# Optimization experiments

Hardware: AMD Instinct MI355X
Metric: run time of the kernel (lower is better)

## Reference

```python
import jax, jax.numpy as jnp
import numpy as np

B, C, H, W = 32, 512, 32, 32
INNER = C // 8


def setup_inputs() -> dict:
    key = jax.random.key(0)
    k_x, k_f, k_g, k_h = jax.random.split(key, 4)
    x = jax.random.normal(k_x, (B, C, H, W), dtype=jnp.float32)
    # 1x1 Conv1d weights (bias=False) are plain [out, in] matrices.
    s_in = 1.0 / np.sqrt(C)
    Wf = jax.random.uniform(k_f, (INNER, C), dtype=jnp.float32, minval=-s_in, maxval=s_in)
    Wg = jax.random.uniform(k_g, (INNER, C), dtype=jnp.float32, minval=-s_in, maxval=s_in)
    Wh = jax.random.uniform(k_h, (C, C), dtype=jnp.float32, minval=-s_in, maxval=s_in)
    return {"x": x, "Wf": Wf, "Wg": Wg, "Wh": Wh}


def reference(x, Wf, Wg, Wh):
    b, c = x.shape[0], x.shape[1]
    xf = x.reshape(b, c, -1)                       # [B, C, N]
    f = jnp.einsum('ic,bcn->bin', Wf, xf)          # [B, inner, N]
    g = jnp.einsum('ic,bcn->bin', Wg, xf)          # [B, inner, N]
    h = jnp.einsum('oc,bcn->bon', Wh, xf)          # [B, C, N]
    sim = jnp.einsum('bin,bim->bnm', f, g)         # f^T g -> [B, N, N]
    beta = jax.nn.softmax(sim, axis=1)             # softmax over the f-index axis (dim=1)
    o = jnp.einsum('bcn,bnm->bcm', h, beta)        # [B, C, N]
    return o
```

## Files before the change

### kernel.cpp

```cpp
#include <hip/hip_runtime.h>
#include <stdint.h>

#define CDIM 512
#define NPIX 1024
#define IDIM 64

#define WS_BATCH (65536 + 65536 + 524288)
#define XT_OFF   ((size_t)32 * WS_BATCH)
#define XT_ELEMS ((size_t)32 * 1024 * 512)
#define WH_OFF   (XT_OFF + XT_ELEMS)
#define P_OFF    XT_OFF
#define P_ELEMS  ((size_t)32 * 1024 * 1024)
#define LP_OFF   (P_OFF + P_ELEMS)

typedef __bf16 bf16x8 __attribute__((ext_vector_type(8)));
typedef _Float16 f16x8 __attribute__((ext_vector_type(8)));
typedef float f32x4 __attribute__((ext_vector_type(4)));

__device__ __forceinline__ unsigned short f2bf(float f) {
    union { float f; uint32_t u; } v; v.f = f;
    uint32_t u = v.u;
    u += 0x7fffu + ((u >> 16) & 1u);
    return (unsigned short)(u >> 16);
}

__device__ __forceinline__ f32x4 mfma_bf(bf16x8 a, bf16x8 b, f32x4 c) {
    return __builtin_amdgcn_mfma_f32_16x16x32_bf16(a, b, c, 0, 0, 0);
}
__device__ __forceinline__ f32x4 mfma_h(f16x8 a, f16x8 b, f32x4 c) {
    return __builtin_amdgcn_mfma_f32_16x16x32_f16(a, b, c, 0, 0, 0);
}
__device__ __forceinline__ void gld_lds16(const void* g, void* l) {
    __builtin_amdgcn_global_load_lds(
        (const __attribute__((address_space(1))) unsigned int*)g,
        (__attribute__((address_space(3))) unsigned int*)l,
        16, 0, 0);
}
__device__ __forceinline__ void barrier_mem() {
    asm volatile("" ::: "memory");
    __builtin_amdgcn_s_barrier();
    asm volatile("" ::: "memory");
}
__device__ __forceinline__ int swz(int by) { return by ^ (((by >> 7) & 3) << 4); }

__global__ __launch_bounds__(256) void wcvt(
    const float* __restrict__ Wf, const float* __restrict__ Wg,
    const float* __restrict__ Wh, _Float16* __restrict__ wh)
{
    int e = (blockIdx.x * 256 + threadIdx.x) * 4;
    int r = e >> 9, k = e & 511;
    const float* src;
    if (r < 64)       src = Wf + (size_t)r * 512 + k;
    else if (r < 128) src = Wg + (size_t)(r - 64) * 512 + k;
    else              src = Wh + (size_t)(r - 128) * 512 + k;
    float4 v = *(const float4*)src;
    _Float16 h4[4] = {(_Float16)v.x, (_Float16)v.y, (_Float16)v.z, (_Float16)v.w};
    *(ushort4*)(wh + e) = *(ushort4*)h4;
}

__global__ __launch_bounds__(256) void xcvt(
    const float* __restrict__ x, _Float16* __restrict__ xT)
{
    __shared__ _Float16 tile[64][72];
    const int b = blockIdx.z, c0 = blockIdx.y * 64, n0 = blockIdx.x * 64;
    const int t = threadIdx.x;
    const float* xb = x + ((size_t)b * CDIM + c0) * NPIX + n0;
    #pragma unroll
    for (int p = 0; p < 4; ++p) {
        int ci = p * 16 + (t >> 4);
        int nj = (t & 15) * 4;
        float4 v = *(const float4*)(xb + (size_t)ci * NPIX + nj);
        tile[nj + 0][ci] = (_Float16)v.x;
        tile[nj + 1][ci] = (_Float16)v.y;
        tile[nj + 2][ci] = (_Float16)v.z;
        tile[nj + 3][ci] = (_Float16)v.w;
    }
    __syncthreads();
    _Float16* dst = xT + ((size_t)b * NPIX + n0) * CDIM + c0;
    #pragma unroll
    for (int p = 0; p < 2; ++p) {
        int n  = p * 32 + (t >> 3);
        int cc = (t & 7) * 8;
        ushort4 a  = *(ushort4*)&tile[n][cc];
        ushort4 bq = *(ushort4*)&tile[n][cc + 4];
        *(ushort4*)(dst + (size_t)n * CDIM + cc)     = a;
        *(ushort4*)(dst + (size_t)n * CDIM + cc + 4) = bq;
    }
}

__global__ __launch_bounds__(256, 4) void fg_mfma(
    const _Float16* __restrict__ wh, const _Float16* __restrict__ xT,
    unsigned short* __restrict__ ws)
{
    const int orig = blockIdx.x;
    const int work = (orig & 7) * 32 + (orig >> 3);
    const int b    = work >> 3;
    const int tn   = work & 7;

    const int t = threadIdx.x, lane = t & 63, w = t >> 6;
    const int lr = lane & 15, lg = lane >> 4;
    const int wr = w >> 1, wc = w & 1;

    __shared__ _Float16 Abuf[2][128 * 32];
    __shared__ _Float16 Bbuf[2][128 * 32];

    const _Float16* Ag = wh;
    const _Float16* Bg = xT + ((size_t)b * NPIX + tn * 128) * CDIM;

    int offA[4], offB[4];
    #pragma unroll
    for (int mf = 0; mf < 4; ++mf)
        offA[mf] = swz((wr * 64 + mf * 16 + lr) * 64 + lg * 16);
    #pragma unroll
    for (int nf = 0; nf < 4; ++nf)
        offB[nf] = swz((wc * 64 + nf * 16 + lr) * 64 + lg * 16);

    f32x4 acc[4][4];
    #pragma unroll
    for (int i = 0; i < 4; ++i)
        #pragma unroll
        for (int j = 0; j < 4; ++j) acc[i][j] = (f32x4){0.f, 0.f, 0.f, 0.f};

    auto stage = [&](int buf, int k0) {
        #pragma unroll
        for (int p = 0; p < 2; ++p) {
            int q = p * 256 + t;
            gld_lds16(Ag + (size_t)(q >> 2) * CDIM + k0 + ((q & 3) ^ ((q >> 3) & 3)) * 8,
                      (char*)&Abuf[buf][0] + q * 16);
        }
        #pragma unroll
        for (int p = 0; p < 2; ++p) {
            int q = p * 256 + t;
            gld_lds16(Bg + (size_t)(q >> 2) * CDIM + k0 + ((q & 3) ^ ((q >> 3) & 3)) * 8,
                      (char*)&Bbuf[buf][0] + q * 16);
        }
    };

    stage(0, 0);
    stage(1, 32);

    #pragma unroll 1
    for (int ks = 0; ks < 16; ++ks) {
        const int cur = ks & 1;
        if (ks < 15) asm volatile("s_waitcnt vmcnt(4)" ::: "memory");
        else         asm volatile("s_waitcnt vmcnt(0)" ::: "memory");
        barrier_mem();

        const char* Ab = (const char*)&Abuf[cur][0];
        const char* Bb = (const char*)&Bbuf[cur][0];
        f16x8 af[4];
        #pragma unroll
        for (int mf = 0; mf < 4; ++mf)
            af[mf] = *(const f16x8*)(Ab + offA[mf]);
        #pragma unroll
        for (int nf = 0; nf < 4; ++nf) {
            f16x8 bv = *(const f16x8*)(Bb + offB[nf]);
            #pragma unroll
            for (int mf = 0; mf < 4; ++mf)
                acc[mf][nf] = mfma_h(af[mf], bv, acc[mf][nf]);
        }

        barrier_mem();
        if (ks + 2 < 16) stage(cur, (ks + 2) * 32);
    }

    unsigned short* base = ws + (size_t)b * WS_BATCH;
    const int nbase = tn * 128 + wc * 64;
    unsigned short* dst = base + (wr ? 65536 : 0);
    #pragma unroll
    for (int mf = 0; mf < 4; ++mf) {
        const int i0 = mf * 16 + lg * 4;
        #pragma unroll
        for (int nf = 0; nf < 4; ++nf) {
            int n = nbase + nf * 16 + lr;
            ushort4 v;
            v.x = f2bf(acc[mf][nf][0]); v.y = f2bf(acc[mf][nf][1]);
            v.z = f2bf(acc[mf][nf][2]); v.w = f2bf(acc[mf][nf][3]);
            *(ushort4*)(dst + (size_t)n * 64 + i0) = v;
        }
    }
}

__global__ __launch_bounds__(512, 2) void h_mfma(
    const _Float16* __restrict__ wh, const _Float16* __restrict__ xT,
    unsigned short* __restrict__ ws)
{
    const int orig = blockIdx.x;
    const int work = (orig & 7) * 32 + (orig >> 3);
    const int b    = work >> 3;
    const int tile = work & 7;
    const int m0   = (tile >> 2) * 256;
    const int n0   = (tile & 3) * 256;

    const int t = threadIdx.x, lane = t & 63, w = t >> 6;
    const int lr = lane & 15, lg = lane >> 4;
    const int wr = w >> 2, wc = w & 3;

    __shared__ __align__(16) char smem[131072];

    const _Float16* Ag = wh + (size_t)(128 + m0) * CDIM;
    const _Float16* Bg = xT + ((size_t)b * NPIX + n0) * CDIM;

    const int sk0 = ((lg) ^ (lr & 7)) * 16;
    const int sk1 = ((4 + lg) ^ (lr & 7)) * 16;
    const int rAbase = (wr * 128 + lr) * 128;
    const int rBbase = (wc * 64 + lr) * 128;

    f32x4 acc[8][4];
    #pragma unroll
    for (int i = 0; i < 8; ++i)
        #pragma unroll
        for (int j = 0; j < 4; ++j) acc[i][j] = (f32x4){0.f, 0.f, 0.f, 0.f};

    auto stage_half = [&](int buf, int isB, int half, int kt) {
        const _Float16* G = isB ? Bg : Ag;
        char* L = smem + isB * 65536 + buf * 32768 + half * 16384;
        #pragma unroll
        for (int l = 0; l < 2; ++l) {
            int q = l * 512 + t;
            gld_lds16(G + (size_t)(half * 128 + (q >> 3)) * CDIM + kt * 64
                        + (((q & 7) ^ ((q >> 3) & 7)) * 8),
                      L + q * 16);
        }
    };

    stage_half(0, 0, 0, 0); stage_half(0, 0, 1, 0);
    stage_half(0, 1, 0, 0); stage_half(0, 1, 1, 0);
    stage_half(1, 1, 0, 1); stage_half(1, 1, 1, 1);
    asm volatile("s_waitcnt vmcnt(4)" ::: "memory");
    barrier_mem();

    f16x8 bfr[4][2];

    #pragma unroll 1
    for (int j = 0; j < 4; ++j) {
        const bool nl = (j < 3);
        #pragma unroll
        for (int grp = 0; grp < 2; ++grp) {
            const char* Abase = smem + grp * 32768;
            const char* Bbase = smem + 65536 + grp * 32768;
            #pragma unroll
            for (int p = 0; p < 4; ++p) {
                if (p == 0) {
                    #pragma unroll
                    for (int nf = 0; nf < 4; ++nf) {
                        bfr[nf][0] = *(const f16x8*)(Bbase + rBbase + nf * 2048 + sk0);
                        bfr[nf][1] = *(const f16x8*)(Bbase + rBbase + nf * 2048 + sk1);
                    }
                }
                f16x8 af[2][2];
                #pragma unroll
                for (int e = 0; e < 2; ++e) {
                    af[e][0] = *(const f16x8*)(Abase + rAbase + (p * 2 + e) * 2048 + sk0);
                    af[e][1] = *(const f16x8*)(Abase + rAbase + (p * 2 + e) * 2048 + sk1);
                }
                if (grp == 0) {
                    if (p == 0) stage_half(1, 0, 0, 2 * j + 1);
                    if (p == 1) stage_half(1, 0, 1, 2 * j + 1);
                    if (p == 2 && nl) stage_half(0, 1, 0, 2 * j + 2);
                    if (p == 3 && nl) stage_half(0, 1, 1, 2 * j + 2);
                } else {
                    if (p == 0 && nl) stage_half(0, 0, 0, 2 * j + 2);
                    if (p == 1 && nl) stage_half(0, 0, 1, 2 * j + 2);
                    if (p == 2 && nl) stage_half(1, 1, 0, 2 * j + 3);
                    if (p == 3 && nl) stage_half(1, 1, 1, 2 * j + 3);
                }
                if (p == 3) {
                    if (nl) asm volatile("s_waitcnt vmcnt(4)" ::: "memory");
                    else    asm volatile("s_waitcnt vmcnt(0)" ::: "memory");
                }
                barrier_mem();
                __builtin_amdgcn_s_setprio(1);
                #pragma unroll
                for (int ks = 0; ks < 2; ++ks)
                    #pragma unroll
                    for (int e = 0; e < 2; ++e)
                        #pragma unroll
                        for (int nf = 0; nf < 4; ++nf)
                            acc[p * 2 + e][nf] =
                                mfma_h(af[e][ks], bfr[nf][ks], acc[p * 2 + e][nf]);
                __builtin_amdgcn_s_setprio(0);
            }
        }
    }

    unsigned short* hd = ws + (size_t)b * WS_BATCH + 131072;
    #pragma unroll
    for (int mf = 0; mf < 8; ++mf)
        #pragma unroll
        for (int nf = 0; nf < 4; ++nf) {
            int n = n0 + wc * 64 + nf * 16 + lr;
            #pragma unroll
            for (int j = 0; j < 4; ++j) {
                int c = m0 + wr * 128 + mf * 16 + lg * 4 + j;
                hd[(size_t)c * NPIX + n] = f2bf(acc[mf][nf][j]);
            }
        }
}

__global__ __launch_bounds__(256, 3) void attn_sm(
    const unsigned short* __restrict__ ws, unsigned short* __restrict__ P,
    float* __restrict__ Lp)
{
    const int orig = blockIdx.x;
    const int work = (orig & 7) * 256 + (orig >> 3);
    const int b    = work >> 6;
    const int tile = work & 63;
    const int mt = tile >> 2, nt = tile & 3;
    const int m0 = mt * 64, n0 = nt * 256;

    const int t = threadIdx.x, lane = t & 63, w = t >> 6;
    const int lr = lane & 15, lg = lane >> 4;

    const unsigned short* fT = ws + (size_t)b * WS_BATCH;
    const unsigned short* gT = fT + 65536;

    __shared__ unsigned short Ab[2][64 * 32];
    __shared__ unsigned short Bb[2][256 * 32];
    __shared__ float red[4][64];
    __shared__ unsigned short rp[4][16][72];

    #pragma unroll
    for (int kc = 0; kc < 2; ++kc) {
        {
            int q = t;
            gld_lds16(gT + (size_t)(m0 + (q >> 2)) * 64 + kc * 32 + ((q & 3) ^ ((q >> 3) & 3)) * 8,
                      (char*)&Ab[kc][0] + q * 16);
        }
        #pragma unroll
        for (int p = 0; p < 4; ++p) {
            int q = p * 256 + t;
            gld_lds16(fT + (size_t)(n0 + (q >> 2)) * 64 + kc * 32 + ((q & 3) ^ ((q >> 3) & 3)) * 8,
                      (char*)&Bb[kc][0] + q * 16);
        }
    }
    __syncthreads();

    int offA[4], offB[4];
    #pragma unroll
    for (int mf = 0; mf < 4; ++mf)
        offA[mf] = swz((mf * 16 + lr) * 64 + lg * 16);
    #pragma unroll
    for (int nf = 0; nf < 4; ++nf)
        offB[nf] = swz((w * 64 + nf * 16 + lr) * 64 + lg * 16);

    f32x4 acc[4][4];
    #pragma unroll
    for (int i = 0; i < 4; ++i)
        #pragma unroll
        for (int j = 0; j < 4; ++j) acc[i][j] = (f32x4){0.f, 0.f, 0.f, 0.f};

    #pragma unroll
    for (int kc = 0; kc < 2; ++kc) {
        const char* Abc = (const char*)&Ab[kc][0];
        const char* Bbc = (const char*)&Bb[kc][0];
        bf16x8 af[4];
        #pragma unroll
        for (int mf = 0; mf < 4; ++mf)
            af[mf] = *(const bf16x8*)(Abc + offA[mf]);
        #pragma unroll
        for (int nf = 0; nf < 4; ++nf) {
            bf16x8 bv = *(const bf16x8*)(Bbc + offB[nf]);
            #pragma unroll
            for (int mf = 0; mf < 4; ++mf)
                acc[mf][nf] = mfma_bf(af[mf], bv, acc[mf][nf]);
        }
    }

    #pragma unroll
    for (int mf = 0; mf < 4; ++mf) {
        #pragma unroll
        for (int j = 0; j < 4; ++j) {
            float s = 0.f;
            #pragma unroll
            for (int nf = 0; nf < 4; ++nf) {
                float e = __expf(acc[mf][nf][j]);
                acc[mf][nf][j] = e;
                s += e;
            }
            s += __shfl_xor(s, 1);
            s += __shfl_xor(s, 2);
            s += __shfl_xor(s, 4);
            s += __shfl_xor(s, 8);
            if (lr == 0) red[w][mf * 16 + lg * 4 + j] = s;
        }
    }
    __syncthreads();
    if (t < 64) {
        float s = red[0][t] + red[1][t] + red[2][t] + red[3][t];
        Lp[(size_t)nt * 32768 + (size_t)b * 1024 + m0 + t] = s;
    }

    unsigned short* Pb = P + (size_t)b * NPIX * NPIX;
    #pragma unroll
    for (int mf = 0; mf < 4; ++mf) {
        #pragma unroll
        for (int nf = 0; nf < 4; ++nf)
            #pragma unroll
            for (int j = 0; j < 4; ++j)
                rp[w][lg * 4 + j][nf * 16 + lr] = f2bf(acc[mf][nf][j]);
        #pragma unroll
        for (int ii = 0; ii < 2; ++ii) {
            int row = ii * 8 + (lane >> 3);
            int ch  = lane & 7;
            ushort4 v0 = *(ushort4*)&rp[w][row][ch * 8];
            ushort4 v1 = *(ushort4*)&rp[w][row][ch * 8 + 4];
            unsigned short* dst = Pb + (size_t)(m0 + mf * 16 + row) * NPIX
                                     + n0 + w * 64 + ch * 8;
            *(ushort4*)(dst)     = v0;
            *(ushort4*)(dst + 4) = v1;
        }
    }
}

__global__ __launch_bounds__(512, 2) void attn_pv(
    const unsigned short* __restrict__ P, const unsigned short* __restrict__ ws,
    const float* __restrict__ Lp, float* __restrict__ out)
{
    const int orig = blockIdx.x;
    const int work = (orig & 7) * 32 + (orig >> 3);
    const int b    = work >> 3;
    const int tile = work & 7;
    const int m0   = (tile >> 1) * 256;
    const int c0   = (tile & 1) * 256;

    const int t = threadIdx.x, lane = t & 63, w = t >> 6;
    const int lr = lane & 15, lg = lane >> 4;
    const int wr = w >> 2, wc = w & 3;

    __shared__ __align__(16) char smem[131072];

    const unsigned short* Ag = P + ((size_t)b * NPIX + m0) * NPIX;
    const unsigned short* Bg = ws + (size_t)b * WS_BATCH + 131072 + (size_t)c0 * NPIX;

    const int sk0 = ((lg) ^ (lr & 7)) * 16;
    const int sk1 = ((4 + lg) ^ (lr & 7)) * 16;
    const int rAbase = (wr * 128 + lr) * 128;
    const int rBbase = (wc * 64 + lr) * 128;

    f32x4 acc[8][4];
    #pragma unroll
    for (int i = 0; i < 8; ++i)
        #pragma unroll
        for (int j = 0; j < 4; ++j) acc[i][j] = (f32x4){0.f, 0.f, 0.f, 0.f};

    auto stage_half = [&](int buf, int isB, int half, int kt) {
        const unsigned short* G = isB ? Bg : Ag;
        char* L = smem + isB * 65536 + buf * 32768 + half * 16384;
        #pragma unroll
        for (int l = 0; l < 2; ++l) {
            int q = l * 512 + t;
            gld_lds16(G + (size_t)(half * 128 + (q >> 3)) * NPIX + kt * 64
                        + (((q & 7) ^ ((q >> 3) & 7)) * 8),
                      L + q * 16);
        }
    };

    stage_half(0, 0, 0, 0); stage_half(0, 0, 1, 0);
    stage_half(0, 1, 0, 0); stage_half(0, 1, 1, 0);
    stage_half(1, 1, 0, 1); stage_half(1, 1, 1, 1);
    asm volatile("s_waitcnt vmcnt(4)" ::: "memory");
    barrier_mem();

    bf16x8 bfr[4][2];

    #pragma unroll 1
    for (int j = 0; j < 8; ++j) {
        const bool nl = (j < 7);
        #pragma unroll
        for (int grp = 0; grp < 2; ++grp) {
            const char* Abase = smem + grp * 32768;
            const char* Bbase = smem + 65536 + grp * 32768;
            #pragma unroll
            for (int p = 0; p < 4; ++p) {
                if (p == 0) {
                    #pragma unroll
                    for (int nf = 0; nf < 4; ++nf) {
                        bfr[nf][0] = *(const bf16x8*)(Bbase + rBbase + nf * 2048 + sk0);
                        bfr[nf][1] = *(const bf16x8*)(Bbase + rBbase + nf * 2048 + sk1);
                    }
                }
                bf16x8 af[2][2];
                #pragma unroll
                for (int e = 0; e < 2; ++e) {
                    af[e][0] = *(const bf16x8*)(Abase + rAbase + (p * 2 + e) * 2048 + sk0);
                    af[e][1] = *(const bf16x8*)(Abase + rAbase + (p * 2 + e) * 2048 + sk1);
                }
                if (grp == 0) {
                    if (p == 0) stage_half(1, 0, 0, 2 * j + 1);
                    if (p == 1) stage_half(1, 0, 1, 2 * j + 1);
                    if (p == 2 && nl) stage_half(0, 1, 0, 2 * j + 2);
                    if (p == 3 && nl) stage_half(0, 1, 1, 2 * j + 2);
                } else {
                    if (p == 0 && nl) stage_half(0, 0, 0, 2 * j + 2);
                    if (p == 1 && nl) stage_half(0, 0, 1, 2 * j + 2);
                    if (p == 2 && nl) stage_half(1, 1, 0, 2 * j + 3);
                    if (p == 3 && nl) stage_half(1, 1, 1, 2 * j + 3);
                }
                if (p == 3) {
                    if (nl) asm volatile("s_waitcnt vmcnt(4)" ::: "memory");
                    else    asm volatile("s_waitcnt vmcnt(0)" ::: "memory");
                }
                barrier_mem();
                __builtin_amdgcn_s_setprio(1);
                #pragma unroll
                for (int ks = 0; ks < 2; ++ks)
                    #pragma unroll
                    for (int e = 0; e < 2; ++e)
                        #pragma unroll
                        for (int nf = 0; nf < 4; ++nf)
                            acc[p * 2 + e][nf] =
                                mfma_bf(af[e][ks], bfr[nf][ks], acc[p * 2 + e][nf]);
                __builtin_amdgcn_s_setprio(0);
            }
        }
    }

    #pragma unroll
    for (int mf = 0; mf < 8; ++mf) {
        const size_t mi = (size_t)b * 1024 + m0 + wr * 128 + mf * 16 + lg * 4;
        f32x4 L = *(const f32x4*)&Lp[mi]
                + *(const f32x4*)&Lp[32768 + mi]
                + *(const f32x4*)&Lp[65536 + mi]
                + *(const f32x4*)&Lp[98304 + mi];
        f32x4 rinv;
        #pragma unroll
        for (int j = 0; j < 4; ++j) rinv[j] = 1.0f / L[j];
        #pragma unroll
        for (int nf = 0; nf < 4; ++nf) {
            f32x4 o = acc[mf][nf] * rinv;
            int c = c0 + wc * 64 + nf * 16 + lr;
            int m = m0 + wr * 128 + mf * 16 + lg * 4;
            *(f32x4*)(out + ((size_t)b * CDIM + c) * NPIX + m) = o;
        }
    }
}

extern "C" void kernel_launch(void* const* d_in, const int* in_sizes, int n_in,
                              void* d_out, int out_size, void* d_ws, size_t ws_size,
                              hipStream_t stream) {
    const float* x  = (const float*)d_in[0];
    const float* Wf = (const float*)d_in[1];
    const float* Wg = (const float*)d_in[2];
    const float* Wh = (const float*)d_in[3];
    unsigned short* ws = (unsigned short*)d_ws;
    _Float16* xT = (_Float16*)(ws + XT_OFF);
    _Float16* wh = (_Float16*)(ws + WH_OFF);
    unsigned short* P = ws + P_OFF;
    float* Lp = (float*)(ws + LP_OFF);
    float* out = (float*)d_out;

    wcvt<<<320, 256, 0, stream>>>(Wf, Wg, Wh, wh);
    xcvt<<<dim3(16, 8, 32), 256, 0, stream>>>(x, xT);
    fg_mfma<<<256, 256, 0, stream>>>(wh, xT, ws);
    h_mfma<<<256, 512, 0, stream>>>(wh, xT, ws);
    attn_sm<<<2048, 256, 0, stream>>>(ws, P, Lp);
    attn_pv<<<256, 512, 0, stream>>>(P, ws, Lp, out);
}
```

Measured before the change: 121.3 us.

## Fuse softmax numerator recompute into PV kernel, eliminating materialized P matrix

The first attention kernel now only computes the column-sum normalizers. The PV kernel recomputes f^T g tiles per 64-pixel chunk, exponentiates them into a shared-memory bf16 tile, and multiplies by h directly. This removes writing and re-reading the full 32x1024x1024 bf16 probability matrix through HBM. In exchange it recomputes the similarity GEMM and exp, uses about 152KB LDS per block (one block per CU), and adds two barriers per K step.

```diff
diff --git a/kernel.cpp b/kernel.cpp
--- a/kernel.cpp
+++ b/kernel.cpp
@@ -9,9 +9,8 @@
 #define XT_OFF   ((size_t)32 * WS_BATCH)
 #define XT_ELEMS ((size_t)32 * 1024 * 512)
 #define WH_OFF   (XT_OFF + XT_ELEMS)
-#define P_OFF    XT_OFF
 #define P_ELEMS  ((size_t)32 * 1024 * 1024)
-#define LP_OFF   (P_OFF + P_ELEMS)
+#define LP_OFF   (XT_OFF + P_ELEMS)
 
 typedef __bf16 bf16x8 __attribute__((ext_vector_type(8)));
 typedef _Float16 f16x8 __attribute__((ext_vector_type(8)));
@@ -298,9 +297,8 @@
         }
 }
 
-__global__ __launch_bounds__(256, 3) void attn_sm(
-    const unsigned short* __restrict__ ws, unsigned short* __restrict__ P,
-    float* __restrict__ Lp)
+__global__ __launch_bounds__(256, 3) void attn_lp(
+    const unsigned short* __restrict__ ws, float* __restrict__ Lp)
 {
     const int orig = blockIdx.x;
     const int work = (orig & 7) * 256 + (orig >> 3);
@@ -318,7 +316,6 @@
     __shared__ unsigned short Ab[2][64 * 32];
     __shared__ unsigned short Bb[2][256 * 32];
     __shared__ float red[4][64];
-    __shared__ unsigned short rp[4][16][72];
 
     #pragma unroll
     for (int kc = 0; kc < 2; ++kc) {
@@ -373,11 +370,8 @@
         for (int j = 0; j < 4; ++j) {
             float s = 0.f;
             #pragma unroll
-            for (int nf = 0; nf < 4; ++nf) {
-                float e = __expf(acc[mf][nf][j]);
-                acc[mf][nf][j] = e;
-                s += e;
-            }
+            for (int nf = 0; nf < 4; ++nf)
+                s += __expf(acc[mf][nf][j]);
             s += __shfl_xor(s, 1);
             s += __shfl_xor(s, 2);
             s += __shfl_xor(s, 4);
@@ -390,32 +384,11 @@
         float s = red[0][t] + red[1][t] + red[2][t] + red[3][t];
         Lp[(size_t)nt * 32768 + (size_t)b * 1024 + m0 + t] = s;
     }
-
-    unsigned short* Pb = P + (size_t)b * NPIX * NPIX;
-    #pragma unroll
-    for (int mf = 0; mf < 4; ++mf) {
-        #pragma unroll
-        for (int nf = 0; nf < 4; ++nf)
-            #pragma unroll
-            for (int j = 0; j < 4; ++j)
-                rp[w][lg * 4 + j][nf * 16 + lr] = f2bf(acc[mf][nf][j]);
-        #pragma unroll
-        for (int ii = 0; ii < 2; ++ii) {
-            int row = ii * 8 + (lane >> 3);
-            int ch  = lane & 7;
-            ushort4 v0 = *(ushort4*)&rp[w][row][ch * 8];
-            ushort4 v1 = *(ushort4*)&rp[w][row][ch * 8 + 4];
-            unsigned short* dst = Pb + (size_t)(m0 + mf * 16 + row) * NPIX
-                                     + n0 + w * 64 + ch * 8;
-            *(ushort4*)(dst)     = v0;
-            *(ushort4*)(dst + 4) = v1;
-        }
-    }
-}
-
-__global__ __launch_bounds__(512, 2) void attn_pv(
-    const unsigned short* __restrict__ P, const unsigned short* __restrict__ ws,
-    const float* __restrict__ Lp, float* __restrict__ out)
+}
+
+__global__ __launch_bounds__(512, 2) void attn_fused(
+    const unsigned short* __restrict__ ws, const float* __restrict__ Lp,
+    float* __restrict__ out)
 {
     const int orig = blockIdx.x;
     const int work = (orig & 7) * 32 + (orig >> 3);
@@ -426,17 +399,18 @@
 
     const int t = threadIdx.x, lane = t & 63, w = t >> 6;
     const int lr = lane & 15, lg = lane >> 4;
-    const int wr = w >> 2, wc = w & 3;
-
-    __shared__ __align__(16) char smem[131072];
-
-    const unsigned short* Ag = P + ((size_t)b * NPIX + m0) * NPIX;
-    const unsigned short* Bg = ws + (size_t)b * WS_BATCH + 131072 + (size_t)c0 * NPIX;
+    const int wr = w >> 2;
+    const int wq = w & 3;
+
+    const unsigned short* fT = ws + (size_t)b * WS_BATCH;
+    const unsigned short* gT = fT + 65536;
+    const unsigned short* hg = fT + 131072;
+
+    __shared__ __align__(16) char smem[155648];
+    unsigned short* Pl = (unsigned short*)(smem + 114688);
 
     const int sk0 = ((lg) ^ (lr & 7)) * 16;
     const int sk1 = ((4 + lg) ^ (lr & 7)) * 16;
-    const int rAbase = (wr * 128 + lr) * 128;
-    const int rBbase = (wc * 64 + lr) * 128;
 
     f32x4 acc[8][4];
     #pragma unroll
@@ -444,76 +418,98 @@
         #pragma unroll
         for (int j = 0; j < 4; ++j) acc[i][j] = (f32x4){0.f, 0.f, 0.f, 0.f};
 
-    auto stage_half = [&](int buf, int isB, int half, int kt) {
-        const unsigned short* G = isB ? Bg : Ag;
-        char* L = smem + isB * 65536 + buf * 32768 + half * 16384;
-        #pragma unroll
-        for (int l = 0; l < 2; ++l) {
+    auto stage_g = [&]() {
+        #pragma unroll
+        for (int l = 0; l < 4; ++l) {
             int q = l * 512 + t;
-            gld_lds16(G + (size_t)(half * 128 + (q >> 3)) * NPIX + kt * 64
-                        + (((q & 7) ^ ((q >> 3) & 7)) * 8),
-                      L + q * 16);
+            gld_lds16(gT + (size_t)(m0 + (q >> 3)) * 64 + (((q & 7) ^ ((q >> 3) & 7)) * 8),
+                      smem + q * 16);
         }
     };
-
-    stage_half(0, 0, 0, 0); stage_half(0, 0, 1, 0);
-    stage_half(0, 1, 0, 0); stage_half(0, 1, 1, 0);
-    stage_half(1, 1, 0, 1); stage_half(1, 1, 1, 1);
-    asm volatile("s_waitcnt vmcnt(4)" ::: "memory");
+    auto stage_f = [&](int buf, int nt) {
+        int q = t;
+        gld_lds16(fT + (size_t)(nt * 64 + (q >> 3)) * 64 + (((q & 7) ^ ((q >> 3) & 7)) * 8),
+                  smem + 32768 + buf * 8192 + q * 16);
+    };
+    auto stage_h = [&](int buf, int nt) {
+        #pragma unroll
+        for (int l = 0; l < 4; ++l) {
+            int q = l * 512 + t;
+            gld_lds16(hg + (size_t)(c0 + (q >> 3)) * NPIX + nt * 64
+                         + (((q & 7) ^ ((q >> 3) & 7)) * 8),
+                      smem + 49152 + buf * 32768 + q * 16);
+        }
+    };
+
+    stage_g();
+    stage_f(0, 0);
+    stage_h(0, 0);
+    stage_f(1, 1);
+    asm volatile("s_waitcnt vmcnt(1)" ::: "memory");
     barrier_mem();
 
-    bf16x8 bfr[4][2];
-
     #pragma unroll 1
-    for (int j = 0; j < 8; ++j) {
-        const bool nl = (j < 7);
-        #pragma unroll
-        for (int grp = 0; grp < 2; ++grp) {
-            const char* Abase = smem + grp * 32768;
-            const char* Bbase = smem + 65536 + grp * 32768;
-            #pragma unroll
-            for (int p = 0; p < 4; ++p) {
-                if (p == 0) {
+    for (int nt = 0; nt < 16; ++nt) {
+        if (nt + 1 < 16) stage_h((nt + 1) & 1, nt + 1);
+
+        const char* fb = smem + 32768 + (nt & 1) * 8192;
+        bf16x8 qb0 = *(const bf16x8*)(fb + (wq * 16 + lr) * 128 + sk0);
+        bf16x8 qb1 = *(const bf16x8*)(fb + (wq * 16 + lr) * 128 + sk1);
+        f32x4 sacc[8];
+        #pragma unroll
+        for (int mf = 0; mf < 8; ++mf) {
+            const char* ga = smem + (wr * 128 + mf * 16 + lr) * 128;
+            bf16x8 a0 = *(const bf16x8*)(ga + sk0);
+            bf16x8 a1 = *(const bf16x8*)(ga + sk1);
+            f32x4 z = {0.f, 0.f, 0.f, 0.f};
+            z = mfma_bf(a0, qb0, z);
+            sacc[mf] = mfma_bf(a1, qb1, z);
+        }
+        #pragma unroll
+        for (int mf = 0; mf < 8; ++mf) {
+            const int row = wr * 128 + mf * 16 + lg * 4;
+            #pragma unroll
+            for (int j = 0; j < 4; ++j)
+                Pl[(row + j) * 80 + wq * 16 + lr] = f2bf(__expf(sacc[mf][j]));
+        }
+        asm volatile("s_waitcnt lgkmcnt(0)" ::: "memory");
+        barrier_mem();
+
+        if (nt + 2 < 16) stage_f(nt & 1, nt + 2);
+
+        if (nt < 14)       asm volatile("s_waitcnt vmcnt(5)" ::: "memory");
+        else if (nt == 14) asm volatile("s_waitcnt vmcnt(4)" ::: "memory");
+        else               asm volatile("s_waitcnt vmcnt(0)" ::: "memory");
+
+        const char* hb_ = smem + 49152 + (nt & 1) * 32768;
+        bf16x8 hb[4][2];
+        #pragma unroll
+        for (int nf = 0; nf < 4; ++nf) {
+            hb[nf][0] = *(const bf16x8*)(hb_ + (wq * 64 + nf * 16 + lr) * 128 + sk0);
+            hb[nf][1] = *(const bf16x8*)(hb_ + (wq * 64 + nf * 16 + lr) * 128 + sk1);
+        }
+        __builtin_amdgcn_s_setprio(1);
+        #pragma unroll
+        for (int p = 0; p < 4; ++p) {
+            bf16x8 af[2][2];
+            #pragma unroll
+            for (int e = 0; e < 2; ++e) {
+                const char* pa = (const char*)Pl + (wr * 128 + (p * 2 + e) * 16 + lr) * 160;
+                af[e][0] = *(const bf16x8*)(pa + lg * 16);
+                af[e][1] = *(const bf16x8*)(pa + 64 + lg * 16);
+            }
+            #pragma unroll
+            for (int ks = 0; ks < 2; ++ks)
+                #pragma unroll
+                for (int e = 0; e < 2; ++e)
                     #pragma unroll
-                    for (int nf = 0; nf < 4; ++nf) {
-                        bfr[nf][0] = *(const bf16x8*)(Bbase + rBbase + nf * 2048 + sk0);
-                        bfr[nf][1] = *(const bf16x8*)(Bbase + rBbase + nf * 2048 + sk1);
-                    }
-                }
-                bf16x8 af[2][2];
-                #pragma unroll
-                for (int e = 0; e < 2; ++e) {
-                    af[e][0] = *(const bf16x8*)(Abase + rAbase + (p * 2 + e) * 2048 + sk0);
-                    af[e][1] = *(const bf16x8*)(Abase + rAbase + (p * 2 + e) * 2048 + sk1);
-                }
-                if (grp == 0) {
-                    if (p == 0) stage_half(1, 0, 0, 2 * j + 1);
-                    if (p == 1) stage_half(1, 0, 1, 2 * j + 1);
-                    if (p == 2 && nl) stage_half(0, 1, 0, 2 * j + 2);
-                    if (p == 3 && nl) stage_half(0, 1, 1, 2 * j + 2);
-                } else {
-                    if (p == 0 && nl) stage_half(0, 0, 0, 2 * j + 2);
-                    if (p == 1 && nl) stage_half(0, 0, 1, 2 * j + 2);
-                    if (p == 2 && nl) stage_half(1, 1, 0, 2 * j + 3);
-                    if (p == 3 && nl) stage_half(1, 1, 1, 2 * j + 3);
-                }
-                if (p == 3) {
-                    if (nl) asm volatile("s_waitcnt vmcnt(4)" ::: "memory");
-                    else    asm volatile("s_waitcnt vmcnt(0)" ::: "memory");
-                }
-                barrier_mem();
-                __builtin_amdgcn_s_setprio(1);
-                #pragma unroll
-                for (int ks = 0; ks < 2; ++ks)
-                    #pragma unroll
-                    for (int e = 0; e < 2; ++e)
-                        #pragma unroll
-                        for (int nf = 0; nf < 4; ++nf)
-                            acc[p * 2 + e][nf] =
-                                mfma_bf(af[e][ks], bfr[nf][ks], acc[p * 2 + e][nf]);
-                __builtin_amdgcn_s_setprio(0);
-            }
-        }
+                    for (int nf = 0; nf < 4; ++nf)
+                        acc[p * 2 + e][nf] =
+                            mfma_bf(af[e][ks], hb[nf][ks], acc[p * 2 + e][nf]);
+        }
+        __builtin_amdgcn_s_setprio(0);
+        asm volatile("s_waitcnt lgkmcnt(0)" ::: "memory");
+        barrier_mem();
     }
 
     #pragma unroll
@@ -529,7 +525,7 @@
         #pragma unroll
         for (int nf = 0; nf < 4; ++nf) {
             f32x4 o = acc[mf][nf] * rinv;
-            int c = c0 + wc * 64 + nf * 16 + lr;
+            int c = c0 + wq * 64 + nf * 16 + lr;
             int m = m0 + wr * 128 + mf * 16 + lg * 4;
             *(f32x4*)(out + ((size_t)b * CDIM + c) * NPIX + m) = o;
         }
@@ -546,7 +542,6 @@
     unsigned short* ws = (unsigned short*)d_ws;
     _Float16* xT = (_Float16*)(ws + XT_OFF);
     _Float16* wh = (_Float16*)(ws + WH_OFF);
-    unsigned short* P = ws + P_OFF;
     float* Lp = (float*)(ws + LP_OFF);
     float* out = (float*)d_out;
 
@@ -554,6 +549,6 @@
     xcvt<<<dim3(16, 8, 32), 256, 0, stream>>>(x, xT);
     fg_mfma<<<256, 256, 0, stream>>>(wh, xT, ws);
     h_mfma<<<256, 512, 0, stream>>>(wh, xT, ws);
-    attn_sm<<<2048, 256, 0, stream>>>(ws, P, Lp);
-    attn_pv<<<256, 512, 0, stream>>>(P, ws, Lp, out);
-}
+    attn_lp<<<2048, 256, 0, stream>>>(ws, Lp);
+    attn_fused<<<256, 512, 0, stream>>>(ws, Lp, out);
+}
```

Result: slower. 130.0 us (+7.1%).

## Merge conversion kernels and fold f/g projection into h GEMM kernel

Applied to the files above, without the earlier changes.

Combines the weight and x conversion kernels into one launch using an extra grid row for weights. Removes the separate f/g GEMM kernel: blocks with tile<4 in the h GEMM kernel compute the f/g projection afterward, reusing shared memory. Also stages the h output through LDS so it is written with 16-byte coalesced stores instead of scattered 2-byte stores. This cuts two launches and improves store efficiency, but adds tail imbalance because half the blocks do extra work.

```diff
diff --git a/kernel.cpp b/kernel.cpp
--- a/kernel.cpp
+++ b/kernel.cpp
@@ -16,6 +16,7 @@
 typedef __bf16 bf16x8 __attribute__((ext_vector_type(8)));
 typedef _Float16 f16x8 __attribute__((ext_vector_type(8)));
 typedef float f32x4 __attribute__((ext_vector_type(4)));
+typedef unsigned short u16x8 __attribute__((ext_vector_type(8)));
 
 __device__ __forceinline__ unsigned short f2bf(float f) {
     union { float f; uint32_t u; } v; v.f = f;
@@ -43,27 +44,29 @@
 }
 __device__ __forceinline__ int swz(int by) { return by ^ (((by >> 7) & 3) << 4); }
 
-__global__ __launch_bounds__(256) void wcvt(
+__global__ __launch_bounds__(256) void xw_cvt(
+    const float* __restrict__ x,
     const float* __restrict__ Wf, const float* __restrict__ Wg,
-    const float* __restrict__ Wh, _Float16* __restrict__ wh)
+    const float* __restrict__ Wh,
+    _Float16* __restrict__ xT, _Float16* __restrict__ wh)
 {
-    int e = (blockIdx.x * 256 + threadIdx.x) * 4;
-    int r = e >> 9, k = e & 511;
-    const float* src;
-    if (r < 64)       src = Wf + (size_t)r * 512 + k;
-    else if (r < 128) src = Wg + (size_t)(r - 64) * 512 + k;
-    else              src = Wh + (size_t)(r - 128) * 512 + k;
-    float4 v = *(const float4*)src;
-    _Float16 h4[4] = {(_Float16)v.x, (_Float16)v.y, (_Float16)v.z, (_Float16)v.w};
-    *(ushort4*)(wh + e) = *(ushort4*)h4;
-}
-
-__global__ __launch_bounds__(256) void xcvt(
-    const float* __restrict__ x, _Float16* __restrict__ xT)
-{
+    const int t = threadIdx.x;
+    if (blockIdx.y == 8) {
+        int wb = blockIdx.z * 16 + blockIdx.x;
+        if (wb >= 320) return;
+        int e = (wb * 256 + t) * 4;
+        int r = e >> 9, k = e & 511;
+        const float* src;
+        if (r < 64)       src = Wf + (size_t)r * 512 + k;
+        else if (r < 128) src = Wg + (size_t)(r - 64) * 512 + k;
+        else              src = Wh + (size_t)(r - 128) * 512 + k;
+        float4 v = *(const float4*)src;
+        _Float16 h4[4] = {(_Float16)v.x, (_Float16)v.y, (_Float16)v.z, (_Float16)v.w};
+        *(ushort4*)(wh + e) = *(ushort4*)h4;
+        return;
+    }
     __shared__ _Float16 tile[64][72];
     const int b = blockIdx.z, c0 = blockIdx.y * 64, n0 = blockIdx.x * 64;
-    const int t = threadIdx.x;
     const float* xb = x + ((size_t)b * CDIM + c0) * NPIX + n0;
     #pragma unroll
     for (int p = 0; p < 4; ++p) {
@@ -88,100 +91,7 @@
     }
 }
 
-__global__ __launch_bounds__(256, 4) void fg_mfma(
-    const _Float16* __restrict__ wh, const _Float16* __restrict__ xT,
-    unsigned short* __restrict__ ws)
-{
-    const int orig = blockIdx.x;
-    const int work = (orig & 7) * 32 + (orig >> 3);
-    const int b    = work >> 3;
-    const int tn   = work & 7;
-
-    const int t = threadIdx.x, lane = t & 63, w = t >> 6;
-    const int lr = lane & 15, lg = lane >> 4;
-    const int wr = w >> 1, wc = w & 1;
-
-    __shared__ _Float16 Abuf[2][128 * 32];
-    __shared__ _Float16 Bbuf[2][128 * 32];
-
-    const _Float16* Ag = wh;
-    const _Float16* Bg = xT + ((size_t)b * NPIX + tn * 128) * CDIM;
-
-    int offA[4], offB[4];
-    #pragma unroll
-    for (int mf = 0; mf < 4; ++mf)
-        offA[mf] = swz((wr * 64 + mf * 16 + lr) * 64 + lg * 16);
-    #pragma unroll
-    for (int nf = 0; nf < 4; ++nf)
-        offB[nf] = swz((wc * 64 + nf * 16 + lr) * 64 + lg * 16);
-
-    f32x4 acc[4][4];
-    #pragma unroll
-    for (int i = 0; i < 4; ++i)
-        #pragma unroll
-        for (int j = 0; j < 4; ++j) acc[i][j] = (f32x4){0.f, 0.f, 0.f, 0.f};
-
-    auto stage = [&](int buf, int k0) {
-        #pragma unroll
-        for (int p = 0; p < 2; ++p) {
-            int q = p * 256 + t;
-            gld_lds16(Ag + (size_t)(q >> 2) * CDIM + k0 + ((q & 3) ^ ((q >> 3) & 3)) * 8,
-                      (char*)&Abuf[buf][0] + q * 16);
-        }
-        #pragma unroll
-        for (int p = 0; p < 2; ++p) {
-            int q = p * 256 + t;
-            gld_lds16(Bg + (size_t)(q >> 2) * CDIM + k0 + ((q & 3) ^ ((q >> 3) & 3)) * 8,
-                      (char*)&Bbuf[buf][0] + q * 16);
-        }
-    };
-
-    stage(0, 0);
-    stage(1, 32);
-
-    #pragma unroll 1
-    for (int ks = 0; ks < 16; ++ks) {
-        const int cur = ks & 1;
-        if (ks < 15) asm volatile("s_waitcnt vmcnt(4)" ::: "memory");
-        else         asm volatile("s_waitcnt vmcnt(0)" ::: "memory");
-        barrier_mem();
-
-        const char* Ab = (const char*)&Abuf[cur][0];
-        const char* Bb = (const char*)&Bbuf[cur][0];
-        f16x8 af[4];
-        #pragma unroll
-        for (int mf = 0; mf < 4; ++mf)
-            af[mf] = *(const f16x8*)(Ab + offA[mf]);
-        #pragma unroll
-        for (int nf = 0; nf < 4; ++nf) {
-            f16x8 bv = *(const f16x8*)(Bb + offB[nf]);
-            #pragma unroll
-            for (int mf = 0; mf < 4; ++mf)
-                acc[mf][nf] = mfma_h(af[mf], bv, acc[mf][nf]);
-        }
-
-        barrier_mem();
-        if (ks + 2 < 16) stage(cur, (ks + 2) * 32);
-    }
-
-    unsigned short* base = ws + (size_t)b * WS_BATCH;
-    const int nbase = tn * 128 + wc * 64;
-    unsigned short* dst = base + (wr ? 65536 : 0);
-    #pragma unroll
-    for (int mf = 0; mf < 4; ++mf) {
-        const int i0 = mf * 16 + lg * 4;
-        #pragma unroll
-        for (int nf = 0; nf < 4; ++nf) {
-            int n = nbase + nf * 16 + lr;
-            ushort4 v;
-            v.x = f2bf(acc[mf][nf][0]); v.y = f2bf(acc[mf][nf][1]);
-            v.z = f2bf(acc[mf][nf][2]); v.w = f2bf(acc[mf][nf][3]);
-            *(ushort4*)(dst + (size_t)n * 64 + i0) = v;
-        }
-    }
-}
-
-__global__ __launch_bounds__(512, 2) void h_mfma(
+__global__ __launch_bounds__(512, 2) void fgh8(
     const _Float16* __restrict__ wh, const _Float16* __restrict__ xT,
     unsigned short* __restrict__ ws)
 {
@@ -284,18 +194,120 @@
         }
     }
 
+    asm volatile("s_waitcnt lgkmcnt(0)" ::: "memory");
+    barrier_mem();
+
     unsigned short* hd = ws + (size_t)b * WS_BATCH + 131072;
-    #pragma unroll
-    for (int mf = 0; mf < 8; ++mf)
-        #pragma unroll
-        for (int nf = 0; nf < 4; ++nf) {
-            int n = n0 + wc * 64 + nf * 16 + lr;
-            #pragma unroll
-            for (int j = 0; j < 4; ++j) {
-                int c = m0 + wr * 128 + mf * 16 + lg * 4 + j;
-                hd[(size_t)c * NPIX + n] = f2bf(acc[mf][nf][j]);
-            }
-        }
+    unsigned short* sc = (unsigned short*)smem + w * 4608;
+    #pragma unroll
+    for (int pass = 0; pass < 2; ++pass) {
+        #pragma unroll
+        for (int mq = 0; mq < 4; ++mq) {
+            const int mf = pass * 4 + mq;
+            #pragma unroll
+            for (int nf = 0; nf < 4; ++nf)
+                #pragma unroll
+                for (int j = 0; j < 4; ++j)
+                    sc[(mq * 16 + lg * 4 + j) * 72 + nf * 16 + lr] =
+                        f2bf(acc[mf][nf][j]);
+        }
+        const int cbase = m0 + wr * 128 + pass * 64;
+        #pragma unroll
+        for (int ii = 0; ii < 8; ++ii) {
+            int cl  = ii * 8 + (lane >> 3);
+            int nl2 = (lane & 7) * 8;
+            u16x8 v = *(const u16x8*)&sc[cl * 72 + nl2];
+            *(u16x8*)(hd + (size_t)(cbase + cl) * NPIX + n0 + wc * 64 + nl2) = v;
+        }
+    }
+
+    if (tile < 4) {
+        asm volatile("s_waitcnt lgkmcnt(0)" ::: "memory");
+        barrier_mem();
+
+        const _Float16* Af = wh;
+        const _Float16* Bf = xT + ((size_t)b * NPIX + tile * 256) * CDIM;
+
+        f32x4 fac[4][4];
+        #pragma unroll
+        for (int i = 0; i < 4; ++i)
+            #pragma unroll
+            for (int j = 0; j < 4; ++j) fac[i][j] = (f32x4){0.f, 0.f, 0.f, 0.f};
+
+        auto stage_fg = [&](int kt) {
+            const int buf = kt & 1;
+            char* La = smem + buf * 16384;
+            char* Lb = smem + 32768 + buf * 32768;
+            #pragma unroll
+            for (int l = 0; l < 2; ++l) {
+                int q = l * 512 + t;
+                gld_lds16(Af + (size_t)(q >> 3) * CDIM + kt * 64
+                            + (((q & 7) ^ ((q >> 3) & 7)) * 8),
+                          La + q * 16);
+            }
+            #pragma unroll
+            for (int l = 0; l < 4; ++l) {
+                int q = l * 512 + t;
+                gld_lds16(Bf + (size_t)(q >> 3) * CDIM + kt * 64
+                            + (((q & 7) ^ ((q >> 3) & 7)) * 8),
+                          Lb + q * 16);
+            }
+        };
+
+        stage_fg(0);
+        stage_fg(1);
+
+        const int rAf = (wr * 64 + lr) * 128;
+
+        #pragma unroll 1
+        for (int kt = 0; kt < 8; ++kt) {
+            if (kt < 7) asm volatile("s_waitcnt vmcnt(6)" ::: "memory");
+            else        asm volatile("s_waitcnt vmcnt(0)" ::: "memory");
+            barrier_mem();
+
+            const char* Ab = smem + (kt & 1) * 16384;
+            const char* Bb = smem + 32768 + (kt & 1) * 32768;
+            f16x8 af[4][2], bf4[4][2];
+            #pragma unroll
+            for (int mf = 0; mf < 4; ++mf) {
+                af[mf][0] = *(const f16x8*)(Ab + rAf + mf * 2048 + sk0);
+                af[mf][1] = *(const f16x8*)(Ab + rAf + mf * 2048 + sk1);
+            }
+            #pragma unroll
+            for (int nf = 0; nf < 4; ++nf) {
+                bf4[nf][0] = *(const f16x8*)(Bb + rBbase + nf * 2048 + sk0);
+                bf4[nf][1] = *(const f16x8*)(Bb + rBbase + nf * 2048 + sk1);
+            }
+            __builtin_amdgcn_s_setprio(1);
+            #pragma unroll
+            for (int ks = 0; ks < 2; ++ks)
+                #pragma unroll
+                for (int mf = 0; mf < 4; ++mf)
+                    #pragma unroll
+                    for (int nf = 0; nf < 4; ++nf)
+                        fac[mf][nf] = mfma_h(af[mf][ks], bf4[nf][ks], fac[mf][nf]);
+            __builtin_amdgcn_s_setprio(0);
+
+            barrier_mem();
+            if (kt + 2 < 8) stage_fg(kt + 2);
+        }
+
+        unsigned short* basefg = ws + (size_t)b * WS_BATCH;
+        unsigned short* dstfg  = basefg + (wr ? 65536 : 0);
+        const int nbasef = tile * 256 + wc * 64;
+        #pragma unroll
+        for (int mf = 0; mf < 4; ++mf) {
+            const int i0 = mf * 16 + lg * 4;
+            #pragma unroll
+            for (int nf = 0; nf < 4; ++nf) {
+                int n = nbasef + nf * 16 + lr;
+                ushort4 v;
+                v.x = f2bf(fac[mf][nf][0]); v.y = f2bf(fac[mf][nf][1]);
+                v.z = f2bf(fac[mf][nf][2]); v.w = f2bf(fac[mf][nf][3]);
+                *(ushort4*)(dstfg + (size_t)n * 64 + i0) = v;
+            }
+        }
+    }
 }
 
 __global__ __launch_bounds__(256, 3) void attn_sm(
@@ -550,10 +562,8 @@
     float* Lp = (float*)(ws + LP_OFF);
     float* out = (float*)d_out;
 
-    wcvt<<<320, 256, 0, stream>>>(Wf, Wg, Wh, wh);
-    xcvt<<<dim3(16, 8, 32), 256, 0, stream>>>(x, xT);
-    fg_mfma<<<256, 256, 0, stream>>>(wh, xT, ws);
-    h_mfma<<<256, 512, 0, stream>>>(wh, xT, ws);
+    xw_cvt<<<dim3(16, 9, 32), 256, 0, stream>>>(x, Wf, Wg, Wh, xT, wh);
+    fgh8<<<256, 512, 0, stream>>>(wh, xT, ws);
     attn_sm<<<2048, 256, 0, stream>>>(ws, P, Lp);
     attn_pv<<<256, 512, 0, stream>>>(P, ws, Lp, out);
 }
```

New measurement: 115.2 us. 1.05x faster.
